# Optimization experiments

Hardware: AMD Instinct MI355X
Metric: run time of the kernel (lower is better)

The kernel has to match this reference:

```python
import jax, jax.numpy as jnp
import numpy as np

S, B, H, R, V = 256, 64, 1024, 512, 512  # seq, batch, hidden, rep(vocab), output


def setup_inputs() -> dict:
    key = jax.random.key(0)
    k = jax.random.split(key, 11)
    n = lambda i, shape, s=0.05: jax.random.normal(k[i], shape, jnp.float32) * s
    return {
        "d_input": n(0, (S, B, R)),
        "cond": jax.random.randint(k[1], (B, 1), 0, 4),
        "e_input": jax.random.randint(k[2], (S, B), 0, R),
        "tf_flag": 1,
        "emb": n(3, (4, H)),
        "W_ih": n(4, (4 * H, R)),
        "W_hh": n(5, (4 * H, H)),
        "b_ih": n(6, (4 * H,)),
        "b_hh": n(7, (4 * H,)),
        "fc_w": n(8, (V, H)),
        "fc_b": n(9, (V,)),
    }


def _lstm_scan(xs, h0, c0, W_ih, W_hh, b_ih, b_hh):
    # xs: [S, B, R]; h0/c0: [B, H]. Torch gate order: i, f, g, o.
    Hd = h0.shape[-1]

    def cell(carry, x_t):
        h, c = carry
        gates = x_t @ W_ih.T + b_ih + h @ W_hh.T + b_hh  # [B, 4H]
        i, f, g, o = jnp.split(gates, 4, axis=-1)
        c = jax.nn.sigmoid(f) * c + jax.nn.sigmoid(i) * jnp.tanh(g)
        h = jax.nn.sigmoid(o) * jnp.tanh(c)
        return (h, c), h

    (h, c), outs = jax.lax.scan(cell, (h0, c0), xs)
    return outs, h, c


def reference(d_input, cond, e_input, tf_flag, emb, W_ih, W_hh, b_ih, b_hh, fc_w, fc_b):
    # cond_embedded = Embedding(cond.T) -> [1, B, H]; repeat over L*D=1 layers
    h0 = emb[cond[:, 0]]  # [B, H]
    c0 = h0
    if tf_flag:
        xs = jax.nn.one_hot(e_input, R, dtype=jnp.float32)  # [S, B, R]
    else:
        xs = d_input
    outs, h, c = _lstm_scan(xs, h0, c0, W_ih, W_hh, b_ih, b_hh)  # outs [S, B, H]
    logits = outs @ fc_w.T + fc_b  # [S, B, V]
    # CrossEntropyLoss(mean) over flattened tokens
    logp = jax.nn.log_softmax(logits.reshape(-1, V), axis=-1)
    labels = e_input.reshape(-1)
    loss = -jnp.mean(jnp.take_along_axis(logp, labels[:, None], axis=-1))
    return (logits, h[None], c[None], loss)
```

## Files before the change

kernel.cpp:

```cpp
#include <hip/hip_runtime.h>
#include <hip/hip_bf16.h>
#include <stdint.h>

#define S_LEN 256
#define BATCH 64
#define HID   1024
#define RDIM  512
#define VOC   512
#define GATES 4096

#define OFF_H    8388608u
#define OFF_C    8454144u
#define OFF_LOSS 8519680u

typedef __attribute__((ext_vector_type(8))) short short8;
typedef __attribute__((ext_vector_type(4))) float f32x4;
typedef __attribute__((ext_vector_type(4))) int   i32x4;
typedef unsigned long long u64;

#define HBUF_BYTES (128u * 1024u)


__device__ inline unsigned short f2bf(float f) {
  unsigned u = __builtin_bit_cast(unsigned, f);
  return (unsigned short)((u + 0x7FFFu + ((u >> 16) & 1u)) >> 16);
}

__device__ inline u64 pack4(float a, float b, float c, float d) {
  return (u64)f2bf(a) | ((u64)f2bf(b) << 16) | ((u64)f2bf(c) << 32) | ((u64)f2bf(d) << 48);
}

__device__ inline f32x4 mfma16(short8 a, short8 b, f32x4 c) {
  return __builtin_amdgcn_mfma_f32_16x16x32_bf16(a, b, c, 0, 0, 0);
}

__device__ inline void stfrag8(char* p, u64 v) {
  __hip_atomic_store((u64*)p, v, __ATOMIC_RELAXED, __HIP_MEMORY_SCOPE_AGENT);
}

__device__ inline size_t fragoff(int b, int hcol) {
  int bt = b >> 4, kk = hcol >> 5;
  int lane = (b & 15) + (((hcol >> 3) & 3) << 4);
  return ((((size_t)bt * 32 + kk) * 64 + lane) << 4) + (size_t)((hcol & 7) * 2);
}

__device__ inline float sigm(float x) {
  return __builtin_amdgcn_rcpf(1.f + __expf(-x));
}
__device__ inline float tanh_(float x) {
  return 1.f - 2.f * __builtin_amdgcn_rcpf(__expf(2.f * x) + 1.f);
}

__global__ void __launch_bounds__(256) k_prep(
    const float* __restrict__ W_ih, const float* __restrict__ b_ih,
    const float* __restrict__ b_hh, const float* __restrict__ fc_w,
    float* __restrict__ T, unsigned short* __restrict__ fcw_bf,
    unsigned* __restrict__ flags, float* __restrict__ loss_slot)
{
  __shared__ float stage[64][65];
  const int bid = blockIdx.x, tid = threadIdx.x;
  if (bid < 512) {
    const int c0 = (bid >> 3) * 64, e0 = (bid & 7) * 64;
    for (int idx = tid; idx < 4096; idx += 256) {
      int i = idx >> 6, jj = idx & 63;
      stage[i][jj] = W_ih[(size_t)(c0 + i) * RDIM + e0 + jj];
    }
    __syncthreads();
    for (int idx = tid; idx < 4096; idx += 256) {
      int jj = idx >> 6, i = idx & 63;
      int c = c0 + i;
      T[(size_t)(e0 + jj) * GATES + c] = stage[i][jj] + b_ih[c] + b_hh[c];
    }
  } else if (bid < 516) {
    const size_t off = (size_t)(bid - 512) * 131072;
    for (int k = tid; k < 32768; k += 256) {
      float4 v = *(const float4*)(fc_w + off + (size_t)k * 4);
      ushort4 o;
      o.x = f2bf(v.x); o.y = f2bf(v.y); o.z = f2bf(v.z); o.w = f2bf(v.w);
      *(ushort4*)(fcw_bf + off + (size_t)k * 4) = o;
    }
  } else {
    for (int k = tid; k < 65536; k += 256)
      __hip_atomic_store(flags + k, 0u, __ATOMIC_RELAXED, __HIP_MEMORY_SCOPE_AGENT);
    if (tid == 0) loss_slot[0] = 0.f;
  }
}

__global__ void __launch_bounds__(256, 1) k_recur(
    const float* __restrict__ W_hh, const float* __restrict__ Tt,
    const int* __restrict__ e_input, const float* __restrict__ emb,
    const int* __restrict__ cond, const float* __restrict__ d_input,
    const int* __restrict__ tf_ptr, const float* __restrict__ W_ih,
    const float* __restrict__ b_ih, const float* __restrict__ b_hh,
    char* __restrict__ hbuf, unsigned* __restrict__ flags,
    unsigned short* __restrict__ outs_r, float* __restrict__ dout)
{
  extern __shared__ char smem[];
  char* Wlds = smem;
  const int j = blockIdx.x;
  const int tid = threadIdx.x;
  const int w = tid >> 6, l = tid & 63;
  const int tf = tf_ptr[0];

  {
    const int nl = tid >> 2;
    const int kq = tid & 3;
    const int g = nl >> 4, hc = nl & 15;
    const float* wrow = W_hh + (size_t)(g * HID + j * 16 + hc) * HID + kq * 256;
    for (int k8 = 0; k8 < 32; ++k8) {
      const int k = kq * 256 + k8 * 8;
      float4 va = *(const float4*)(wrow + k8 * 8);
      float4 vb = *(const float4*)(wrow + k8 * 8 + 4);
      u64 lo = pack4(va.x, va.y, va.z, va.w);
      u64 hi = pack4(vb.x, vb.y, vb.z, vb.w);
      const int kk = k >> 5;
      const int lane = (nl & 15) + (((k >> 3) & 3) << 4);
      char* p = Wlds + (((size_t)(g * 32 + kk) * 64 + lane) << 4);
      *(u64*)p = lo;
      *(u64*)(p + 8) = hi;
    }
  }

  const int b = w * 16 + (l & 15);
  const int hcl = (l >> 4) * 4;
  const int hcol = j * 16 + hcl;
  float cr[4];
  {
    const int cd = cond[b];
    float4 h0 = *(const float4*)(emb + (size_t)cd * HID + hcol);
    cr[0] = h0.x; cr[1] = h0.y; cr[2] = h0.z; cr[3] = h0.w;
    stfrag8(hbuf + fragoff(b, hcol), pack4(h0.x, h0.y, h0.z, h0.w));
  }
  asm volatile("s_waitcnt vmcnt(0)" ::: "memory");
  __syncthreads();
  if (tid == 0)
    __hip_atomic_store(flags + j, 1u, __ATOMIC_RELAXED, __HIP_MEMORY_SCOPE_AGENT);

#define MFMA_BT(bt)                                                           \
  _Pragma("unroll")                                                           \
  for (int kkl = 0; kkl < 8; ++kkl) {                                         \
    const int kk = (bt) * 8 + kkl;                                            \
    _Pragma("unroll")                                                         \
    for (int nt = 0; nt < 4; ++nt) {                                          \
      short8 Wv = *(const short8*)(Wlds + ((((size_t)nt * 32 + kk) * 64 + l) << 4)); \
      acc[nt] = mfma16(Wv, __builtin_bit_cast(short8, a[kk]), acc[nt]);       \
    }                                                                         \
  }

  for (int t = 0; t < S_LEN; ++t) {
    float4 t0, t1, t2, t3;
    if (tf != 0) {
      const float* Trow = Tt + (size_t)e_input[t * BATCH + b] * GATES;
      t0 = *(const float4*)(Trow + 0 * HID + hcol);
      t1 = *(const float4*)(Trow + 1 * HID + hcol);
      t2 = *(const float4*)(Trow + 2 * HID + hcol);
      t3 = *(const float4*)(Trow + 3 * HID + hcol);
    }

    if (tid < 64) {
      const unsigned* fp = flags + (size_t)t * 64 + tid;
      int guard = 0;
      while (__hip_atomic_load(fp, __ATOMIC_RELAXED, __HIP_MEMORY_SCOPE_AGENT) == 0u) {
        __builtin_amdgcn_s_sleep(1);
        if (++guard > (1 << 24)) break;
      }
    }
    __syncthreads();

    const char* hbl = hbuf + (size_t)(t & 1) * HBUF_BYTES
                      + (((size_t)w * 32 * 64 + l) << 4);
    i32x4 a[32];
#pragma unroll
    for (int kk = 0; kk < 32; ++kk) {
      asm volatile("global_load_dwordx4 %0, %1, off sc0 sc1"
                   : "=v"(a[kk]) : "v"(hbl + (size_t)kk * 1024));
    }
    f32x4 acc[4];
    acc[0] = {0.f, 0.f, 0.f, 0.f}; acc[1] = {0.f, 0.f, 0.f, 0.f};
    acc[2] = {0.f, 0.f, 0.f, 0.f}; acc[3] = {0.f, 0.f, 0.f, 0.f};
    asm volatile("s_waitcnt vmcnt(24)" ::: "memory");
    __builtin_amdgcn_sched_barrier(0);
    MFMA_BT(0)
    asm volatile("s_waitcnt vmcnt(16)" ::: "memory");
    __builtin_amdgcn_sched_barrier(0);
    MFMA_BT(1)
    asm volatile("s_waitcnt vmcnt(8)" ::: "memory");
    __builtin_amdgcn_sched_barrier(0);
    MFMA_BT(2)
    asm volatile("s_waitcnt vmcnt(0)" ::: "memory");
    __builtin_amdgcn_sched_barrier(0);
    MFMA_BT(3)

    float gq[4][4];
#pragma unroll
    for (int g = 0; g < 4; ++g)
#pragma unroll
      for (int r = 0; r < 4; ++r)
        gq[g][r] = acc[g][r];
    if (tf != 0) {
      gq[0][0] += t0.x; gq[0][1] += t0.y; gq[0][2] += t0.z; gq[0][3] += t0.w;
      gq[1][0] += t1.x; gq[1][1] += t1.y; gq[1][2] += t1.z; gq[1][3] += t1.w;
      gq[2][0] += t2.x; gq[2][1] += t2.y; gq[2][2] += t2.z; gq[2][3] += t2.w;
      gq[3][0] += t3.x; gq[3][1] += t3.y; gq[3][2] += t3.z; gq[3][3] += t3.w;
    } else {
      const float* x = d_input + ((size_t)t * BATCH + b) * RDIM;
#pragma unroll
      for (int g = 0; g < 4; ++g)
#pragma unroll
        for (int r = 0; r < 4; ++r) {
          const int row = g * HID + hcol + r;
          const float* wr = W_ih + (size_t)row * RDIM;
          float s = b_ih[row] + b_hh[row];
          for (int k = 0; k < RDIM; ++k) s += x[k] * wr[k];
          gq[g][r] += s;
        }
    }
    float hnew[4];
#pragma unroll
    for (int r = 0; r < 4; ++r) {
      float ig = sigm(gq[0][r]);
      float fg = sigm(gq[1][r]);
      float gg = tanh_(gq[2][r]);
      float og = sigm(gq[3][r]);
      cr[r] = fg * cr[r] + ig * gg;
      hnew[r] = og * tanh_(cr[r]);
    }
    const u64 pk = pack4(hnew[0], hnew[1], hnew[2], hnew[3]);
    stfrag8(hbuf + (size_t)((t + 1) & 1) * HBUF_BYTES + fragoff(b, hcol), pk);
    *(u64*)(outs_r + (size_t)j * 262144 + ((size_t)t * BATCH + b) * 16 + hcl) = pk;
    if (t == S_LEN - 1) {
      *(float4*)(dout + OFF_H + (size_t)b * HID + hcol) = make_float4(hnew[0], hnew[1], hnew[2], hnew[3]);
      *(float4*)(dout + OFF_C + (size_t)b * HID + hcol) = make_float4(cr[0], cr[1], cr[2], cr[3]);
    }
    asm volatile("s_waitcnt vmcnt(0)" ::: "memory");
    __syncthreads();
    if (tid == 0 && t < S_LEN - 1)
      __hip_atomic_store(flags + (size_t)(t + 1) * 64 + j, 1u,
                         __ATOMIC_RELAXED, __HIP_MEMORY_SCOPE_AGENT);
  }
#undef MFMA_BT
}

__global__ void __launch_bounds__(256) k_gemm(
    const unsigned short* __restrict__ A,
    const unsigned short* __restrict__ Bw,
    const float* __restrict__ fcb, float* __restrict__ C)
{
  const int bid = blockIdx.x;
  const int m0 = (bid >> 3) * 64, n0 = (bid & 7) * 64;
  const int tid = threadIdx.x, w = tid >> 6, l = tid & 63;
  const int mt0 = (w >> 1) * 2, nt0 = (w & 1) * 2;
  f32x4 acc[2][2];
  acc[0][0] = {0.f, 0.f, 0.f, 0.f}; acc[0][1] = {0.f, 0.f, 0.f, 0.f};
  acc[1][0] = {0.f, 0.f, 0.f, 0.f}; acc[1][1] = {0.f, 0.f, 0.f, 0.f};
  const int ksel  = (l >> 4) & 3;
  const int jsel  = ksel >> 1;
  const int koffL = (ksel & 1) * 8;
  const int m_a0 = m0 + mt0 * 16 + (l & 15);
  const unsigned short* a0p = A + (size_t)jsel * 262144 + (size_t)m_a0 * 16 + koffL;
  const unsigned short* a1p = a0p + 16 * 16;
  const int koff = ksel * 8;
  const unsigned short* b0p = Bw + (size_t)(n0 + nt0 * 16 + (l & 15)) * HID + koff;
  const unsigned short* b1p = b0p + 16 * HID;
#pragma unroll 4
  for (int kk = 0; kk < 32; ++kk) {
    short8 A0 = *(const short8*)(a0p + (size_t)kk * 524288);
    short8 A1 = *(const short8*)(a1p + (size_t)kk * 524288);
    short8 B0 = *(const short8*)(b0p + kk * 32);
    short8 B1 = *(const short8*)(b1p + kk * 32);
    acc[0][0] = mfma16(A0, B0, acc[0][0]);
    acc[0][1] = mfma16(A0, B1, acc[0][1]);
    acc[1][0] = mfma16(A1, B0, acc[1][0]);
    acc[1][1] = mfma16(A1, B1, acc[1][1]);
  }
  const int rb = (l >> 4) * 4, cb = l & 15;
#pragma unroll
  for (int i2 = 0; i2 < 2; ++i2)
#pragma unroll
    for (int j2 = 0; j2 < 2; ++j2) {
      const int n = n0 + (nt0 + j2) * 16 + cb;
      const float fb = fcb[n];
#pragma unroll
      for (int r = 0; r < 4; ++r) {
        const int m = m0 + (mt0 + i2) * 16 + rb + r;
        C[(size_t)m * VOC + n] = acc[i2][j2][r] + fb;
      }
    }
}

__global__ void __launch_bounds__(256) k_loss(
    const float* __restrict__ logits, const int* __restrict__ labels,
    float* __restrict__ dout)
{
  const int tid = threadIdx.x, w = tid >> 6, l = tid & 63;
  float part = 0.f;
  for (int i = 0; i < 16; ++i) {
    const int row = blockIdx.x * 64 + w * 16 + i;
    const float* lr = logits + (size_t)row * VOC;
    float4 x0 = *(const float4*)(lr + l * 8);
    float4 x1 = *(const float4*)(lr + l * 8 + 4);
    float v[8] = {x0.x, x0.y, x0.z, x0.w, x1.x, x1.y, x1.z, x1.w};
    float mx = v[0];
#pragma unroll
    for (int k = 1; k < 8; ++k) mx = fmaxf(mx, v[k]);
    for (int off = 32; off; off >>= 1) mx = fmaxf(mx, __shfl_xor(mx, off));
    float se = 0.f;
#pragma unroll
    for (int k = 0; k < 8; ++k) se += __expf(v[k] - mx);
    for (int off = 32; off; off >>= 1) se += __shfl_xor(se, off);
    const float lse = mx + __logf(se);
    const int lab = labels[row];
    const int li = lab - l * 8;
    float pick = v[0];
#pragma unroll
    for (int k = 1; k < 8; ++k) pick = (li == k) ? v[k] : pick;
    float term = (li >= 0 && li < 8) ? (lse - pick) : 0.f;
    for (int off = 32; off; off >>= 1) term += __shfl_xor(term, off);
    part += term;
  }
  if (l == 0) atomicAdd(dout + OFF_LOSS, part * (1.f / 16384.f));
}

extern "C" void kernel_launch(void* const* d_in, const int* in_sizes, int n_in,
                              void* d_out, int out_size, void* d_ws, size_t ws_size,
                              hipStream_t stream) {
  const float* d_input = (const float*)d_in[0];
  const int*   cond    = (const int*)d_in[1];
  const int*   e_input = (const int*)d_in[2];
  const int*   tf_ptr  = (const int*)d_in[3];
  const float* emb     = (const float*)d_in[4];
  const float* W_ih    = (const float*)d_in[5];
  const float* W_hh    = (const float*)d_in[6];
  const float* b_ih    = (const float*)d_in[7];
  const float* b_hh    = (const float*)d_in[8];
  const float* fc_w    = (const float*)d_in[9];
  const float* fc_b    = (const float*)d_in[10];
  float* out = (float*)d_out;
  char*  ws  = (char*)d_ws;

  const size_t WS_T    = 0;
  const size_t WS_FCW  = 8388608;
  const size_t WS_OUTS = 9437184;
  const size_t WS_HBUF = 42991616;
  const size_t WS_FLAG = WS_HBUF + 2ull * HBUF_BYTES;
  char* hbuf = ws + WS_HBUF;
  unsigned* flags = (unsigned*)(ws + WS_FLAG);
  float* T = (float*)(ws + WS_T);
  unsigned short* fcw  = (unsigned short*)(ws + WS_FCW);
  unsigned short* outs = (unsigned short*)(ws + WS_OUTS);

  hipFuncSetAttribute((const void*)k_recur,
                      hipFuncAttributeMaxDynamicSharedMemorySize, 131072);

  k_prep<<<dim3(517), dim3(256), 0, stream>>>(W_ih, b_ih, b_hh, fc_w, T, fcw,
                                              flags, out + OFF_LOSS);
  k_recur<<<dim3(64), dim3(256), 131072, stream>>>(
      W_hh, T, e_input, emb, cond, d_input, tf_ptr, W_ih, b_ih, b_hh,
      hbuf, flags, outs, out);
  k_gemm<<<dim3(2048), dim3(256), 0, stream>>>(outs, fcw, fc_b, out);
  k_loss<<<dim3(256), dim3(256), 0, stream>>>(out, e_input, out);
}
```

Measured before the change: 1.429 ms.

## Run LSTM recurrence with one wavefront per block and double-buffered h loads

Shrinks the persistent recurrence kernel from four wavefronts to a single wavefront per block. That one wave now handles all 64 batch rows and all four gates, so the per-step __syncthreads barriers go away and each lane spins on its own flag. The h-state loads are streamed in 16 chunks through two ping-pong register buffers, and the embedding-table lookups plus the outs store are moved off the critical path until after the MFMA loop and the flag publish. The cost is four times as much MFMA and load work serialized in one wave per CU, with higher register pressure.

After: 3.775 ms. +164.1%, slower.

```diff
diff --git a/kernel.cpp b/kernel.cpp
--- a/kernel.cpp
+++ b/kernel.cpp
@@ -86,7 +86,7 @@
   }
 }
 
-__global__ void __launch_bounds__(256, 1) k_recur(
+__global__ void __launch_bounds__(64, 1) k_recur(
     const float* __restrict__ W_hh, const float* __restrict__ Tt,
     const int* __restrict__ e_input, const float* __restrict__ emb,
     const int* __restrict__ cond, const float* __restrict__ d_input,
@@ -98,147 +98,166 @@
   extern __shared__ char smem[];
   char* Wlds = smem;
   const int j = blockIdx.x;
-  const int tid = threadIdx.x;
-  const int w = tid >> 6, l = tid & 63;
+  const int l = threadIdx.x;
   const int tf = tf_ptr[0];
 
-  {
-    const int nl = tid >> 2;
-    const int kq = tid & 3;
-    const int g = nl >> 4, hc = nl & 15;
-    const float* wrow = W_hh + (size_t)(g * HID + j * 16 + hc) * HID + kq * 256;
-    for (int k8 = 0; k8 < 32; ++k8) {
-      const int k = kq * 256 + k8 * 8;
-      float4 va = *(const float4*)(wrow + k8 * 8);
-      float4 vb = *(const float4*)(wrow + k8 * 8 + 4);
-      u64 lo = pack4(va.x, va.y, va.z, va.w);
-      u64 hi = pack4(vb.x, vb.y, vb.z, vb.w);
-      const int kk = k >> 5;
-      const int lane = (nl & 15) + (((k >> 3) & 3) << 4);
-      char* p = Wlds + (((size_t)(g * 32 + kk) * 64 + lane) << 4);
-      *(u64*)p = lo;
-      *(u64*)(p + 8) = hi;
-    }
-  }
-
-  const int b = w * 16 + (l & 15);
+  for (int idx = l; idx < 8192; idx += 64) {
+    const int g = idx >> 11, kk = (idx >> 6) & 31, lane = idx & 63;
+    const float* wr = W_hh + (size_t)(g * HID + j * 16 + (lane & 15)) * HID
+                      + kk * 32 + ((lane >> 4) & 3) * 8;
+    float4 va = *(const float4*)wr;
+    float4 vb = *(const float4*)(wr + 4);
+    char* p = Wlds + (((size_t)(g * 32 + kk) * 64 + lane) << 4);
+    *(u64*)p = pack4(va.x, va.y, va.z, va.w);
+    *(u64*)(p + 8) = pack4(vb.x, vb.y, vb.z, vb.w);
+  }
+
   const int hcl = (l >> 4) * 4;
   const int hcol = j * 16 + hcl;
-  float cr[4];
-  {
+  f32x4 cr[4];
+#pragma unroll
+  for (int bt = 0; bt < 4; ++bt) {
+    const int b = bt * 16 + (l & 15);
     const int cd = cond[b];
     float4 h0 = *(const float4*)(emb + (size_t)cd * HID + hcol);
-    cr[0] = h0.x; cr[1] = h0.y; cr[2] = h0.z; cr[3] = h0.w;
+    cr[bt][0] = h0.x; cr[bt][1] = h0.y; cr[bt][2] = h0.z; cr[bt][3] = h0.w;
     stfrag8(hbuf + fragoff(b, hcol), pack4(h0.x, h0.y, h0.z, h0.w));
   }
   asm volatile("s_waitcnt vmcnt(0)" ::: "memory");
   __syncthreads();
-  if (tid == 0)
+  if (l == 0)
     __hip_atomic_store(flags + j, 1u, __ATOMIC_RELAXED, __HIP_MEMORY_SCOPE_AGENT);
 
-#define MFMA_BT(bt)                                                           \
+#define ISSUE(buf, c)                                                         \
+  _Pragma("unroll")                                                           \
+  for (int q = 0; q < 8; ++q)                                                 \
+    asm volatile("global_load_dwordx4 %0, %1, off sc0 sc1"                    \
+                 : "=v"(buf[q])                                               \
+                 : "v"(hbl + (size_t)(c) * 8192 + (size_t)q * 1024));
+
+#define W8  asm volatile("s_waitcnt vmcnt(8)" ::: "memory"); __builtin_amdgcn_sched_barrier(0);
+#define W0  asm volatile("s_waitcnt vmcnt(0)" ::: "memory"); __builtin_amdgcn_sched_barrier(0);
+
+#define CHUNK(cc, buf)                                                        \
   _Pragma("unroll")                                                           \
   for (int kkl = 0; kkl < 8; ++kkl) {                                         \
-    const int kk = (bt) * 8 + kkl;                                            \
+    const int kk = ((cc) & 3) * 8 + kkl;                                      \
     _Pragma("unroll")                                                         \
-    for (int nt = 0; nt < 4; ++nt) {                                          \
-      short8 Wv = *(const short8*)(Wlds + ((((size_t)nt * 32 + kk) * 64 + l) << 4)); \
-      acc[nt] = mfma16(Wv, __builtin_bit_cast(short8, a[kk]), acc[nt]);       \
+    for (int g = 0; g < 4; ++g) {                                             \
+      short8 Wv = *(const short8*)(Wlds + ((((size_t)g * 32 + kk) * 64 + l) << 4)); \
+      acc[(cc) >> 2][g] = mfma16(Wv, __builtin_bit_cast(short8, buf[kkl]),    \
+                                 acc[(cc) >> 2][g]);                          \
     }                                                                         \
   }
 
   for (int t = 0; t < S_LEN; ++t) {
-    float4 t0, t1, t2, t3;
+    int e[4];
     if (tf != 0) {
-      const float* Trow = Tt + (size_t)e_input[t * BATCH + b] * GATES;
-      t0 = *(const float4*)(Trow + 0 * HID + hcol);
-      t1 = *(const float4*)(Trow + 1 * HID + hcol);
-      t2 = *(const float4*)(Trow + 2 * HID + hcol);
-      t3 = *(const float4*)(Trow + 3 * HID + hcol);
-    }
-
-    if (tid < 64) {
-      const unsigned* fp = flags + (size_t)t * 64 + tid;
+#pragma unroll
+      for (int bt = 0; bt < 4; ++bt)
+        e[bt] = e_input[t * BATCH + bt * 16 + (l & 15)];
+    }
+
+    {
+      const unsigned* fp = flags + (size_t)t * 64 + l;
       int guard = 0;
       while (__hip_atomic_load(fp, __ATOMIC_RELAXED, __HIP_MEMORY_SCOPE_AGENT) == 0u) {
         __builtin_amdgcn_s_sleep(1);
         if (++guard > (1 << 24)) break;
       }
     }
-    __syncthreads();
-
-    const char* hbl = hbuf + (size_t)(t & 1) * HBUF_BYTES
-                      + (((size_t)w * 32 * 64 + l) << 4);
-    i32x4 a[32];
-#pragma unroll
-    for (int kk = 0; kk < 32; ++kk) {
-      asm volatile("global_load_dwordx4 %0, %1, off sc0 sc1"
-                   : "=v"(a[kk]) : "v"(hbl + (size_t)kk * 1024));
-    }
-    f32x4 acc[4];
-    acc[0] = {0.f, 0.f, 0.f, 0.f}; acc[1] = {0.f, 0.f, 0.f, 0.f};
-    acc[2] = {0.f, 0.f, 0.f, 0.f}; acc[3] = {0.f, 0.f, 0.f, 0.f};
-    asm volatile("s_waitcnt vmcnt(24)" ::: "memory");
-    __builtin_amdgcn_sched_barrier(0);
-    MFMA_BT(0)
-    asm volatile("s_waitcnt vmcnt(16)" ::: "memory");
-    __builtin_amdgcn_sched_barrier(0);
-    MFMA_BT(1)
-    asm volatile("s_waitcnt vmcnt(8)" ::: "memory");
-    __builtin_amdgcn_sched_barrier(0);
-    MFMA_BT(2)
     asm volatile("s_waitcnt vmcnt(0)" ::: "memory");
     __builtin_amdgcn_sched_barrier(0);
-    MFMA_BT(3)
-
-    float gq[4][4];
-#pragma unroll
-    for (int g = 0; g < 4; ++g)
-#pragma unroll
-      for (int r = 0; r < 4; ++r)
-        gq[g][r] = acc[g][r];
+
+    const char* hbl = hbuf + (size_t)(t & 1) * HBUF_BYTES + (size_t)l * 16;
+    i32x4 bufA[8], bufB[8];
+    f32x4 acc[4][4];
+#pragma unroll
+    for (int bt = 0; bt < 4; ++bt)
+#pragma unroll
+      for (int g = 0; g < 4; ++g)
+        acc[bt][g] = (f32x4){0.f, 0.f, 0.f, 0.f};
+    ISSUE(bufA, 0) ISSUE(bufB, 1)
+    W8 CHUNK(0, bufA)  ISSUE(bufA, 2)
+    W8 CHUNK(1, bufB)  ISSUE(bufB, 3)
+    W8 CHUNK(2, bufA)  ISSUE(bufA, 4)
+    W8 CHUNK(3, bufB)  ISSUE(bufB, 5)
+    W8 CHUNK(4, bufA)  ISSUE(bufA, 6)
+    W8 CHUNK(5, bufB)  ISSUE(bufB, 7)
+    W8 CHUNK(6, bufA)  ISSUE(bufA, 8)
+    W8 CHUNK(7, bufB)  ISSUE(bufB, 9)
+    W8 CHUNK(8, bufA)  ISSUE(bufA, 10)
+    W8 CHUNK(9, bufB)  ISSUE(bufB, 11)
+    W8 CHUNK(10, bufA) ISSUE(bufA, 12)
+    W8 CHUNK(11, bufB) ISSUE(bufB, 13)
+    W8 CHUNK(12, bufA) ISSUE(bufA, 14)
+    W8 CHUNK(13, bufB) ISSUE(bufB, 15)
+    W8 CHUNK(14, bufA)
+    W0 CHUNK(15, bufB)
+
+    f32x4 tg[4][4];
     if (tf != 0) {
-      gq[0][0] += t0.x; gq[0][1] += t0.y; gq[0][2] += t0.z; gq[0][3] += t0.w;
-      gq[1][0] += t1.x; gq[1][1] += t1.y; gq[1][2] += t1.z; gq[1][3] += t1.w;
-      gq[2][0] += t2.x; gq[2][1] += t2.y; gq[2][2] += t2.z; gq[2][3] += t2.w;
-      gq[3][0] += t3.x; gq[3][1] += t3.y; gq[3][2] += t3.z; gq[3][3] += t3.w;
+#pragma unroll
+      for (int bt = 0; bt < 4; ++bt) {
+        const float* Trow = Tt + (size_t)e[bt] * GATES;
+#pragma unroll
+        for (int g = 0; g < 4; ++g)
+          tg[bt][g] = *(const f32x4*)(Trow + g * HID + hcol);
+      }
     } else {
-      const float* x = d_input + ((size_t)t * BATCH + b) * RDIM;
-#pragma unroll
-      for (int g = 0; g < 4; ++g)
-#pragma unroll
-        for (int r = 0; r < 4; ++r) {
-          const int row = g * HID + hcol + r;
-          const float* wr = W_ih + (size_t)row * RDIM;
-          float s = b_ih[row] + b_hh[row];
-          for (int k = 0; k < RDIM; ++k) s += x[k] * wr[k];
-          gq[g][r] += s;
-        }
-    }
-    float hnew[4];
-#pragma unroll
-    for (int r = 0; r < 4; ++r) {
-      float ig = sigm(gq[0][r]);
-      float fg = sigm(gq[1][r]);
-      float gg = tanh_(gq[2][r]);
-      float og = sigm(gq[3][r]);
-      cr[r] = fg * cr[r] + ig * gg;
-      hnew[r] = og * tanh_(cr[r]);
-    }
-    const u64 pk = pack4(hnew[0], hnew[1], hnew[2], hnew[3]);
-    stfrag8(hbuf + (size_t)((t + 1) & 1) * HBUF_BYTES + fragoff(b, hcol), pk);
-    *(u64*)(outs_r + (size_t)j * 262144 + ((size_t)t * BATCH + b) * 16 + hcl) = pk;
-    if (t == S_LEN - 1) {
-      *(float4*)(dout + OFF_H + (size_t)b * HID + hcol) = make_float4(hnew[0], hnew[1], hnew[2], hnew[3]);
-      *(float4*)(dout + OFF_C + (size_t)b * HID + hcol) = make_float4(cr[0], cr[1], cr[2], cr[3]);
+#pragma unroll
+      for (int bt = 0; bt < 4; ++bt) {
+        const int b = bt * 16 + (l & 15);
+        const float* x = d_input + ((size_t)t * BATCH + b) * RDIM;
+#pragma unroll
+        for (int g = 0; g < 4; ++g)
+          for (int r = 0; r < 4; ++r) {
+            const int row = g * HID + hcol + r;
+            const float* wr = W_ih + (size_t)row * RDIM;
+            float s = b_ih[row] + b_hh[row];
+            for (int k = 0; k < RDIM; ++k) s += x[k] * wr[k];
+            tg[bt][g][r] = s;
+          }
+      }
+    }
+
+    u64 pk[4];
+#pragma unroll
+    for (int bt = 0; bt < 4; ++bt) {
+      const int b = bt * 16 + (l & 15);
+      float hnew[4];
+#pragma unroll
+      for (int r = 0; r < 4; ++r) {
+        float ig = sigm(acc[bt][0][r] + tg[bt][0][r]);
+        float fg = sigm(acc[bt][1][r] + tg[bt][1][r]);
+        float gg = tanh_(acc[bt][2][r] + tg[bt][2][r]);
+        float og = sigm(acc[bt][3][r] + tg[bt][3][r]);
+        cr[bt][r] = fg * cr[bt][r] + ig * gg;
+        hnew[r] = og * tanh_(cr[bt][r]);
+      }
+      pk[bt] = pack4(hnew[0], hnew[1], hnew[2], hnew[3]);
+      stfrag8(hbuf + (size_t)((t + 1) & 1) * HBUF_BYTES + fragoff(b, hcol), pk[bt]);
+      if (t == S_LEN - 1) {
+        *(float4*)(dout + OFF_H + (size_t)b * HID + hcol) =
+            make_float4(hnew[0], hnew[1], hnew[2], hnew[3]);
+        *(float4*)(dout + OFF_C + (size_t)b * HID + hcol) =
+            make_float4(cr[bt][0], cr[bt][1], cr[bt][2], cr[bt][3]);
+      }
     }
     asm volatile("s_waitcnt vmcnt(0)" ::: "memory");
-    __syncthreads();
-    if (tid == 0 && t < S_LEN - 1)
+    if (l == 0 && t < S_LEN - 1)
       __hip_atomic_store(flags + (size_t)(t + 1) * 64 + j, 1u,
                          __ATOMIC_RELAXED, __HIP_MEMORY_SCOPE_AGENT);
-  }
-#undef MFMA_BT
+#pragma unroll
+    for (int bt = 0; bt < 4; ++bt) {
+      const int b = bt * 16 + (l & 15);
+      *(u64*)(outs_r + (size_t)j * 262144 + ((size_t)t * BATCH + b) * 16 + hcl) = pk[bt];
+    }
+  }
+#undef ISSUE
+#undef W8
+#undef W0
+#undef CHUNK
 }
 
 __global__ void __launch_bounds__(256) k_gemm(
@@ -354,7 +373,7 @@
 
   k_prep<<<dim3(517), dim3(256), 0, stream>>>(W_ih, b_ih, b_hh, fc_w, T, fcw,
                                               flags, out + OFF_LOSS);
-  k_recur<<<dim3(64), dim3(256), 131072, stream>>>(
+  k_recur<<<dim3(64), dim3(64), 131072, stream>>>(
       W_hh, T, e_input, emb, cond, d_input, tf_ptr, W_ih, b_ih, b_hh,
       hbuf, flags, outs, out);
   k_gemm<<<dim3(2048), dim3(256), 0, stream>>>(outs, fcw, fc_b, out);
```

## Split recurrent matmul K across waves and use per-wave byte flags

Applied to the files above, without the earlier changes.

Each wave now computes half of the K dimension for two batch tiles, and the partial sums are exchanged through LDS as bf16 and added before the gate math. Step completion is signalled with per-wave byte flags, so the block-wide barrier before the flag store is gone and consumers wait until all four bytes are set. The outs store is moved after the flag signal to shorten the critical path. The cost is an extra LDS round trip and barrier per step, and partial sums rounded to bf16 lose some precision.

After: 2.061 ms. 44.2% more time.

```diff
diff --git a/kernel.cpp b/kernel.cpp
--- a/kernel.cpp
+++ b/kernel.cpp
@@ -28,6 +28,10 @@
 
 __device__ inline u64 pack4(float a, float b, float c, float d) {
   return (u64)f2bf(a) | ((u64)f2bf(b) << 16) | ((u64)f2bf(c) << 32) | ((u64)f2bf(d) << 48);
+}
+
+__device__ inline float bfx(u64 v, int sh) {
+  return __builtin_bit_cast(float, (unsigned)(((unsigned)(v >> sh) & 0xFFFFu) << 16));
 }
 
 __device__ inline f32x4 mfma16(short8 a, short8 b, f32x4 c) {
@@ -80,7 +84,7 @@
       *(ushort4*)(fcw_bf + off + (size_t)k * 4) = o;
     }
   } else {
-    for (int k = tid; k < 65536; k += 256)
+    for (int k = tid; k < 16384; k += 256)
       __hip_atomic_store(flags + k, 0u, __ATOMIC_RELAXED, __HIP_MEMORY_SCOPE_AGENT);
     if (tid == 0) loss_slot[0] = 0.f;
   }
@@ -97,9 +101,12 @@
 {
   extern __shared__ char smem[];
   char* Wlds = smem;
+  u64* pbuf = (u64*)(smem + 131072);
   const int j = blockIdx.x;
   const int tid = threadIdx.x;
   const int w = tid >> 6, l = tid & 63;
+  const int kh = w & 1, bp = w >> 1;
+  const int kbase = kh * 16;
   const int tf = tf_ptr[0];
 
   {
@@ -133,17 +140,31 @@
   }
   asm volatile("s_waitcnt vmcnt(0)" ::: "memory");
   __syncthreads();
-  if (tid == 0)
-    __hip_atomic_store(flags + j, 1u, __ATOMIC_RELAXED, __HIP_MEMORY_SCOPE_AGENT);
-
-#define MFMA_BT(bt)                                                           \
+  if (l == 0)
+    __hip_atomic_store((unsigned char*)(flags + j) + w, (unsigned char)1,
+                       __ATOMIC_RELAXED, __HIP_MEMORY_SCOPE_AGENT);
+
+#define ISSUE_OCT(buf, oct)                                                   \
+  _Pragma("unroll")                                                           \
+  for (int q = 0; q < 8; ++q)                                                 \
+    asm volatile("global_load_dwordx4 %0, %1, off sc0 sc1"                    \
+                 : "=v"(buf[q])                                               \
+                 : "v"(hbl + (((size_t)(2 * bp) * 32 + kbase + (oct) * 8 + q) << 10))); \
+  _Pragma("unroll")                                                           \
+  for (int q = 0; q < 8; ++q)                                                 \
+    asm volatile("global_load_dwordx4 %0, %1, off sc0 sc1"                    \
+                 : "=v"(buf[8 + q])                                           \
+                 : "v"(hbl + (((size_t)(2 * bp + 1) * 32 + kbase + (oct) * 8 + q) << 10)));
+
+#define CHUNK(oct, buf)                                                       \
   _Pragma("unroll")                                                           \
   for (int kkl = 0; kkl < 8; ++kkl) {                                         \
-    const int kk = (bt) * 8 + kkl;                                            \
+    const int kk = kbase + (oct) * 8 + kkl;                                   \
     _Pragma("unroll")                                                         \
     for (int nt = 0; nt < 4; ++nt) {                                          \
       short8 Wv = *(const short8*)(Wlds + ((((size_t)nt * 32 + kk) * 64 + l) << 4)); \
-      acc[nt] = mfma16(Wv, __builtin_bit_cast(short8, a[kk]), acc[nt]);       \
+      acc0[nt] = mfma16(Wv, __builtin_bit_cast(short8, buf[kkl]), acc0[nt]);  \
+      acc1[nt] = mfma16(Wv, __builtin_bit_cast(short8, buf[8 + kkl]), acc1[nt]); \
     }                                                                         \
   }
 
@@ -160,43 +181,50 @@
     if (tid < 64) {
       const unsigned* fp = flags + (size_t)t * 64 + tid;
       int guard = 0;
-      while (__hip_atomic_load(fp, __ATOMIC_RELAXED, __HIP_MEMORY_SCOPE_AGENT) == 0u) {
+      while (__hip_atomic_load(fp, __ATOMIC_RELAXED, __HIP_MEMORY_SCOPE_AGENT)
+             != 0x01010101u) {
         __builtin_amdgcn_s_sleep(1);
         if (++guard > (1 << 24)) break;
       }
     }
     __syncthreads();
-
-    const char* hbl = hbuf + (size_t)(t & 1) * HBUF_BYTES
-                      + (((size_t)w * 32 * 64 + l) << 4);
-    i32x4 a[32];
-#pragma unroll
-    for (int kk = 0; kk < 32; ++kk) {
-      asm volatile("global_load_dwordx4 %0, %1, off sc0 sc1"
-                   : "=v"(a[kk]) : "v"(hbl + (size_t)kk * 1024));
-    }
-    f32x4 acc[4];
-    acc[0] = {0.f, 0.f, 0.f, 0.f}; acc[1] = {0.f, 0.f, 0.f, 0.f};
-    acc[2] = {0.f, 0.f, 0.f, 0.f}; acc[3] = {0.f, 0.f, 0.f, 0.f};
-    asm volatile("s_waitcnt vmcnt(24)" ::: "memory");
+    asm volatile("s_waitcnt vmcnt(0)" ::: "memory");
     __builtin_amdgcn_sched_barrier(0);
-    MFMA_BT(0)
+
+    const char* hbl = hbuf + (size_t)(t & 1) * HBUF_BYTES + (size_t)l * 16;
+    i32x4 bufA[16], bufB[16];
+    f32x4 acc0[4], acc1[4];
+    acc0[0] = {0.f,0.f,0.f,0.f}; acc0[1] = {0.f,0.f,0.f,0.f};
+    acc0[2] = {0.f,0.f,0.f,0.f}; acc0[3] = {0.f,0.f,0.f,0.f};
+    acc1[0] = {0.f,0.f,0.f,0.f}; acc1[1] = {0.f,0.f,0.f,0.f};
+    acc1[2] = {0.f,0.f,0.f,0.f}; acc1[3] = {0.f,0.f,0.f,0.f};
+    ISSUE_OCT(bufA, 0)
+    ISSUE_OCT(bufB, 1)
     asm volatile("s_waitcnt vmcnt(16)" ::: "memory");
     __builtin_amdgcn_sched_barrier(0);
-    MFMA_BT(1)
-    asm volatile("s_waitcnt vmcnt(8)" ::: "memory");
-    __builtin_amdgcn_sched_barrier(0);
-    MFMA_BT(2)
+    CHUNK(0, bufA)
     asm volatile("s_waitcnt vmcnt(0)" ::: "memory");
     __builtin_amdgcn_sched_barrier(0);
-    MFMA_BT(3)
+    CHUNK(1, bufB)
+
+#pragma unroll
+    for (int nt = 0; nt < 4; ++nt) {
+      pbuf[(((size_t)kh * 4 + 2 * bp) * 4 + nt) * 64 + l] =
+          pack4(acc0[nt][0], acc0[nt][1], acc0[nt][2], acc0[nt][3]);
+      pbuf[(((size_t)kh * 4 + 2 * bp + 1) * 4 + nt) * 64 + l] =
+          pack4(acc1[nt][0], acc1[nt][1], acc1[nt][2], acc1[nt][3]);
+    }
+    __syncthreads();
 
     float gq[4][4];
 #pragma unroll
-    for (int g = 0; g < 4; ++g)
+    for (int g = 0; g < 4; ++g) {
+      const u64 p0 = pbuf[(((size_t)0 * 4 + w) * 4 + g) * 64 + l];
+      const u64 p1 = pbuf[(((size_t)1 * 4 + w) * 4 + g) * 64 + l];
 #pragma unroll
       for (int r = 0; r < 4; ++r)
-        gq[g][r] = acc[g][r];
+        gq[g][r] = bfx(p0, r * 16) + bfx(p1, r * 16);
+    }
     if (tf != 0) {
       gq[0][0] += t0.x; gq[0][1] += t0.y; gq[0][2] += t0.z; gq[0][3] += t0.w;
       gq[1][0] += t1.x; gq[1][1] += t1.y; gq[1][2] += t1.z; gq[1][3] += t1.w;
@@ -227,18 +255,19 @@
     }
     const u64 pk = pack4(hnew[0], hnew[1], hnew[2], hnew[3]);
     stfrag8(hbuf + (size_t)((t + 1) & 1) * HBUF_BYTES + fragoff(b, hcol), pk);
-    *(u64*)(outs_r + (size_t)j * 262144 + ((size_t)t * BATCH + b) * 16 + hcl) = pk;
     if (t == S_LEN - 1) {
       *(float4*)(dout + OFF_H + (size_t)b * HID + hcol) = make_float4(hnew[0], hnew[1], hnew[2], hnew[3]);
       *(float4*)(dout + OFF_C + (size_t)b * HID + hcol) = make_float4(cr[0], cr[1], cr[2], cr[3]);
     }
     asm volatile("s_waitcnt vmcnt(0)" ::: "memory");
-    __syncthreads();
-    if (tid == 0 && t < S_LEN - 1)
-      __hip_atomic_store(flags + (size_t)(t + 1) * 64 + j, 1u,
+    if (l == 0 && t < S_LEN - 1)
+      __hip_atomic_store((unsigned char*)(flags + (size_t)(t + 1) * 64 + j) + w,
+                         (unsigned char)1,
                          __ATOMIC_RELAXED, __HIP_MEMORY_SCOPE_AGENT);
-  }
-#undef MFMA_BT
+    *(u64*)(outs_r + (size_t)j * 262144 + ((size_t)t * BATCH + b) * 16 + hcl) = pk;
+  }
+#undef ISSUE_OCT
+#undef CHUNK
 }
 
 __global__ void __launch_bounds__(256) k_gemm(
@@ -349,12 +378,13 @@
   unsigned short* fcw  = (unsigned short*)(ws + WS_FCW);
   unsigned short* outs = (unsigned short*)(ws + WS_OUTS);
 
+  const int ldsz = 131072 + 16384;
   hipFuncSetAttribute((const void*)k_recur,
-                      hipFuncAttributeMaxDynamicSharedMemorySize, 131072);
+                      hipFuncAttributeMaxDynamicSharedMemorySize, ldsz);
 
   k_prep<<<dim3(517), dim3(256), 0, stream>>>(W_ih, b_ih, b_hh, fc_w, T, fcw,
                                               flags, out + OFF_LOSS);
-  k_recur<<<dim3(64), dim3(256), 131072, stream>>>(
+  k_recur<<<dim3(64), dim3(256), ldsz, stream>>>(
       W_hh, T, e_input, emb, cond, d_input, tf_ptr, W_ih, b_ih, b_hh,
       hbuf, flags, outs, out);
   k_gemm<<<dim3(2048), dim3(256), 0, stream>>>(outs, fcw, fc_b, out);
```

## Replace block-wide step barrier with per-wave byte flags and chunked waits

Applied to the files above, without the earlier changes.

Each wave now publishes its own byte flag per timestep instead of one block-level flag after __syncthreads. Consumers poll per-wave flags with a ballot and issue each 8-load chunk of the hidden state as soon as its 16 producer blocks are ready, so loads overlap with the remaining waits. The outs store is moved after the flag publish to shorten the critical path. This drops two block barriers per step, but each lane now spins on its own flag, which adds atomic polling traffic. Ordering also now depends on per-wave vmcnt waits.

New measurement: 2.582 ms. 1.81x slower.

```diff
diff --git a/kernel.cpp b/kernel.cpp
--- a/kernel.cpp
+++ b/kernel.cpp
@@ -132,9 +132,17 @@
     stfrag8(hbuf + fragoff(b, hcol), pack4(h0.x, h0.y, h0.z, h0.w));
   }
   asm volatile("s_waitcnt vmcnt(0)" ::: "memory");
+  if (l == 0)
+    __hip_atomic_store((unsigned char*)(flags + j) + w, (unsigned char)1,
+                       __ATOMIC_RELAXED, __HIP_MEMORY_SCOPE_AGENT);
   __syncthreads();
-  if (tid == 0)
-    __hip_atomic_store(flags + j, 1u, __ATOMIC_RELAXED, __HIP_MEMORY_SCOPE_AGENT);
+
+#define ISSUE(c)                                                              \
+  _Pragma("unroll")                                                           \
+  for (int q = 0; q < 8; ++q)                                                 \
+    asm volatile("global_load_dwordx4 %0, %1, off sc0 sc1"                    \
+                 : "=v"(a[(c) * 8 + q])                                       \
+                 : "v"(hbl + (size_t)((c) * 8 + q) * 1024));
 
 #define MFMA_BT(bt)                                                           \
   _Pragma("unroll")                                                           \
@@ -157,24 +165,28 @@
       t3 = *(const float4*)(Trow + 3 * HID + hcol);
     }
 
-    if (tid < 64) {
-      const unsigned* fp = flags + (size_t)t * 64 + tid;
-      int guard = 0;
-      while (__hip_atomic_load(fp, __ATOMIC_RELAXED, __HIP_MEMORY_SCOPE_AGENT) == 0u) {
-        __builtin_amdgcn_s_sleep(1);
+    const unsigned char* fb = (const unsigned char*)(flags + (size_t)t * 64 + l) + w;
+    u64 seen = 0;
+    bool mine = false;
+    int guard = 0;
+    auto waitchunk = [&](int c) {
+      const u64 m = 0xFFFFull << (16 * c);
+      while ((seen & m) != m) {
+        if (!mine)
+          mine = (__hip_atomic_load(fb, __ATOMIC_RELAXED,
+                                    __HIP_MEMORY_SCOPE_AGENT) != 0);
+        seen = __ballot(mine);
         if (++guard > (1 << 24)) break;
       }
-    }
-    __syncthreads();
+    };
 
     const char* hbl = hbuf + (size_t)(t & 1) * HBUF_BYTES
                       + (((size_t)w * 32 * 64 + l) << 4);
     i32x4 a[32];
-#pragma unroll
-    for (int kk = 0; kk < 32; ++kk) {
-      asm volatile("global_load_dwordx4 %0, %1, off sc0 sc1"
-                   : "=v"(a[kk]) : "v"(hbl + (size_t)kk * 1024));
-    }
+    waitchunk(0); ISSUE(0)
+    waitchunk(1); ISSUE(1)
+    waitchunk(2); ISSUE(2)
+    waitchunk(3); ISSUE(3)
     f32x4 acc[4];
     acc[0] = {0.f, 0.f, 0.f, 0.f}; acc[1] = {0.f, 0.f, 0.f, 0.f};
     acc[2] = {0.f, 0.f, 0.f, 0.f}; acc[3] = {0.f, 0.f, 0.f, 0.f};
@@ -227,17 +239,18 @@
     }
     const u64 pk = pack4(hnew[0], hnew[1], hnew[2], hnew[3]);
     stfrag8(hbuf + (size_t)((t + 1) & 1) * HBUF_BYTES + fragoff(b, hcol), pk);
-    *(u64*)(outs_r + (size_t)j * 262144 + ((size_t)t * BATCH + b) * 16 + hcl) = pk;
     if (t == S_LEN - 1) {
       *(float4*)(dout + OFF_H + (size_t)b * HID + hcol) = make_float4(hnew[0], hnew[1], hnew[2], hnew[3]);
       *(float4*)(dout + OFF_C + (size_t)b * HID + hcol) = make_float4(cr[0], cr[1], cr[2], cr[3]);
     }
     asm volatile("s_waitcnt vmcnt(0)" ::: "memory");
-    __syncthreads();
-    if (tid == 0 && t < S_LEN - 1)
-      __hip_atomic_store(flags + (size_t)(t + 1) * 64 + j, 1u,
+    if (l == 0 && t < S_LEN - 1)
+      __hip_atomic_store((unsigned char*)(flags + (size_t)(t + 1) * 64 + j) + w,
+                         (unsigned char)1,
                          __ATOMIC_RELAXED, __HIP_MEMORY_SCOPE_AGENT);
-  }
+    *(u64*)(outs_r + (size_t)j * 262144 + ((size_t)t * BATCH + b) * 16 + hcl) = pk;
+  }
+#undef ISSUE
 #undef MFMA_BT
 }
 
```
